# Kernel optimization log

Hardware: AMD Instinct MI355X
Metric: run time of the kernel (lower is better)

## Reference

```python
import jax, jax.numpy as jnp
import numpy as np
import math

# Instant-NGP hash-grid encoding constants (from HashEncodingConfig)
L = 16          # number of levels
LOG_T = 19
T = 2 ** LOG_T  # hash table size per level
F = 2           # features per entry
N_MIN = 16
N_MAX = 512
X_MIN = 0.0
X_MAX = 1.0
P = 2 ** 21     # number of query points

_scaler = math.exp((math.log(N_MAX) - math.log(N_MIN)) / (L - 1))
RESOLUTIONS = [int(N_MIN * _scaler ** i) for i in range(L)]

# 8 corner offsets of a voxel, shape [8, 3]
CORNER_OFFS = np.array([[i, j, k] for i in (0, 1) for j in (0, 1) for k in (0, 1)], dtype=np.int32)
# spatial hashing primes (tiny-cuda-nn / Instant-NGP)
PRIMES = np.array([1, 2654435761, 805459861], dtype=np.uint32)


def setup_inputs() -> dict:
    key = jax.random.key(0)
    kx, kh = jax.random.split(key)
    x = jax.random.uniform(kx, (P, 3), dtype=jnp.float32)  # points in [0,1]^3
    hashmap = jax.random.normal(kh, (L, T, F), dtype=jnp.float32) * 1e-4
    return {"x": x, "hashmap": hashmap}


def _encode_level(x, table, res):
    # x: [P,3] in [0,1]; table: [T,F]; res: python int
    xs = x * res                              # [P,3]
    xi = jnp.floor(xs).astype(jnp.int32)      # [P,3] integer cell
    xf = xs - xi.astype(xs.dtype)             # [P,3] fractional part
    corners = (xi[:, None, :] + CORNER_OFFS[None]).astype(jnp.uint32)  # [P,8,3]
    h = (corners[..., 0] * PRIMES[0]) ^ (corners[..., 1] * PRIMES[1]) ^ (corners[..., 2] * PRIMES[2])
    idx = (h & jnp.uint32(T - 1)).astype(jnp.int32)                     # [P,8]
    feats = table[idx]                                                  # [P,8,F] gather
    # trilinear weights: prod over 3 dims of xf (offset=1) or 1-xf (offset=0)
    w = jnp.prod(jnp.where(CORNER_OFFS[None].astype(bool), xf[:, None, :], 1.0 - xf[:, None, :]), axis=-1)  # [P,8]
    return jnp.sum(feats * w[..., None], axis=1)                        # [P,F]


def reference(x, hashmap):
    xn = (x - X_MIN) / (X_MAX - X_MIN)
    outs = [_encode_level(xn, hashmap[l], RESOLUTIONS[l]) for l in range(L)]
    return jnp.concatenate(outs, axis=-1)  # [P, L*F]
```

## Files before the change

kernel.cpp:

```cpp
#include <hip/hip_runtime.h>
#include <cstdint>
#include <cstddef>

namespace {
constexpr int kL = 16;
constexpr uint32_t kT = 1u << 19;
constexpr uint32_t kTmask = kT - 1u;
constexpr uint32_t kP1 = 2654435761u;
constexpr uint32_t kP2 = 805459861u;
}

struct Prep {
    uint32_t idx[8];
    float w[8];
};

__device__ __forceinline__ void prep_point(float px, float py, float pz,
                                           float fres, Prep& pr) {
    const float xs0 = px * fres;
    const float xs1 = py * fres;
    const float xs2 = pz * fres;
    const float fl0 = floorf(xs0);
    const float fl1 = floorf(xs1);
    const float fl2 = floorf(xs2);
    const float fx = xs0 - fl0;
    const float fy = xs1 - fl1;
    const float fz = xs2 - fl2;
    const uint32_t i0 = (uint32_t)(int)fl0;
    const uint32_t i1 = (uint32_t)(int)fl1;
    const uint32_t i2 = (uint32_t)(int)fl2;

    const uint32_t h0a = i0;
    const uint32_t h0b = i0 + 1u;
    const uint32_t h1a = i1 * kP1;
    const uint32_t h1b = (i1 + 1u) * kP1;
    const uint32_t h2a = i2 * kP2;
    const uint32_t h2b = (i2 + 1u) * kP2;

    pr.idx[0] = (h0a ^ h1a ^ h2a) & kTmask;
    pr.idx[1] = (h0a ^ h1a ^ h2b) & kTmask;
    pr.idx[2] = (h0a ^ h1b ^ h2a) & kTmask;
    pr.idx[3] = (h0a ^ h1b ^ h2b) & kTmask;
    pr.idx[4] = (h0b ^ h1a ^ h2a) & kTmask;
    pr.idx[5] = (h0b ^ h1a ^ h2b) & kTmask;
    pr.idx[6] = (h0b ^ h1b ^ h2a) & kTmask;
    pr.idx[7] = (h0b ^ h1b ^ h2b) & kTmask;

    const float wx0 = 1.0f - fx, wx1 = fx;
    const float wy0 = 1.0f - fy, wy1 = fy;
    const float wz0 = 1.0f - fz, wz1 = fz;
    pr.w[0] = wx0 * wy0 * wz0;
    pr.w[1] = wx0 * wy0 * wz1;
    pr.w[2] = wx0 * wy1 * wz0;
    pr.w[3] = wx0 * wy1 * wz1;
    pr.w[4] = wx1 * wy0 * wz0;
    pr.w[5] = wx1 * wy0 * wz1;
    pr.w[6] = wx1 * wy1 * wz0;
    pr.w[7] = wx1 * wy1 * wz1;
}

__device__ __forceinline__ uint32_t f32_to_bf16_rne(float f) {
    const uint32_t u = __float_as_uint(f);
    return (u + 0x7fffu + ((u >> 16) & 1u)) >> 16;
}

__global__ __launch_bounds__(256) void convert_tables(
    const float4* __restrict__ hm4,
    uint2* __restrict__ tbl_bf,
    int npairs)
{
    const int i = blockIdx.x * 256 + threadIdx.x;
    if (i >= npairs) return;
    const float4 v = hm4[i];
    uint2 o;
    o.x = (f32_to_bf16_rne(v.y) << 16) | f32_to_bf16_rne(v.x);
    o.y = (f32_to_bf16_rne(v.w) << 16) | f32_to_bf16_rne(v.z);
    tbl_bf[i] = o;
}

__global__ __launch_bounds__(256) void hashgrid_levels(
    const float* __restrict__ x,
    const uint32_t* __restrict__ tbl_bf,
    uint32_t* __restrict__ wsb,
    int P, int blocksPerLevel)
{
    const int l = blockIdx.x / blocksPerLevel;
    const int b = blockIdx.x - l * blocksPerLevel;
    const int t = b * 256 + threadIdx.x;
    const int p0 = 2 * t;
    if (p0 >= P) return;

    const int oct = (l * 11) >> 5;
    const int rem = l - 3 * oct;
    const float base = (float)(16 << oct);
    const float cmul = (rem == 0) ? 1.0f : ((rem == 1) ? 1.2599210499f : 1.5874010520f);
    const float fres = (float)(int)(base * cmul);

    const float* __restrict__ xp = x + (size_t)p0 * 3;
    const float ax = xp[0], ay = xp[1], az = xp[2];
    const float bx = xp[3], by = xp[4], bz = xp[5];

    Prep A, B;
    prep_point(ax, ay, az, fres, A);
    prep_point(bx, by, bz, fres, B);

    const uint32_t* __restrict__ tbl = tbl_bf + (size_t)l * (size_t)kT;

    uint32_t ua[8], ub[8];
#pragma unroll
    for (int c = 0; c < 8; ++c) ua[c] = tbl[A.idx[c]];
#pragma unroll
    for (int c = 0; c < 8; ++c) ub[c] = tbl[B.idx[c]];

    float a0 = 0.0f, a1 = 0.0f, b0 = 0.0f, b1 = 0.0f;
#pragma unroll
    for (int c = 0; c < 8; ++c) {
        a0 = fmaf(A.w[c], __uint_as_float(ua[c] << 16), a0);
        a1 = fmaf(A.w[c], __uint_as_float(ua[c] & 0xffff0000u), a1);
        b0 = fmaf(B.w[c], __uint_as_float(ub[c] << 16), b0);
        b1 = fmaf(B.w[c], __uint_as_float(ub[c] & 0xffff0000u), b1);
    }

    const uint32_t pa = (f32_to_bf16_rne(a1) << 16) | f32_to_bf16_rne(a0);
    const uint32_t pb = (f32_to_bf16_rne(b1) << 16) | f32_to_bf16_rne(b0);

    uint32_t* dst = wsb + (size_t)l * (size_t)P + (size_t)p0;
    if (p0 + 1 < P) {
        *reinterpret_cast<uint2*>(dst) = make_uint2(pa, pb);
    } else {
        *dst = pa;
    }
}

__global__ __launch_bounds__(256) void hashgrid_transpose(
    const uint32_t* __restrict__ wsb,
    float4* __restrict__ out4,
    int P)
{
    __shared__ uint32_t lds[256 * 17];
    const int tid = threadIdx.x;
    const int base = blockIdx.x * 256;

#pragma unroll
    for (int l = 0; l < kL; ++l) {
        const int p = base + tid;
        const uint32_t v = (p < P) ? wsb[(size_t)l * (size_t)P + (size_t)p] : 0u;
        lds[tid * 17 + l] = v;
    }
    __syncthreads();

    const int nvec = min(P - base, 256) * 8;
#pragma unroll
    for (int j = 0; j < 8; ++j) {
        const int tvec = j * 256 + tid;
        if (tvec < nvec) {
            const int pl = tvec >> 3;
            const int m = tvec & 7;
            const uint32_t ua = lds[pl * 17 + 2 * m];
            const uint32_t ub = lds[pl * 17 + 2 * m + 1];
            out4[(size_t)base * 8 + (size_t)tvec] =
                make_float4(__uint_as_float(ua << 16),
                            __uint_as_float(ua & 0xffff0000u),
                            __uint_as_float(ub << 16),
                            __uint_as_float(ub & 0xffff0000u));
        }
    }
}

__global__ __launch_bounds__(256) void hashgrid_fwd_mono(
    const float* __restrict__ x,
    const float* __restrict__ hashmap,
    float4* __restrict__ out4,
    int P)
{
    constexpr int RES[16] = {16, 20, 25, 32, 40, 50, 64, 80,
                             101, 128, 161, 203, 256, 322, 406, 512};
    const int p = blockIdx.x * 256 + threadIdx.x;
    if (p >= P) return;
    const float px = x[p * 3 + 0];
    const float py = x[p * 3 + 1];
    const float pz = x[p * 3 + 2];
    float acc[32];
#pragma unroll
    for (int l = 0; l < kL; ++l) {
        Prep pr;
        prep_point(px, py, pz, (float)RES[l], pr);
        const float2* __restrict__ tbl =
            reinterpret_cast<const float2*>(hashmap) + (size_t)l * (size_t)kT;
        float2 f[8];
#pragma unroll
        for (int c = 0; c < 8; ++c) f[c] = tbl[pr.idx[c]];
        float a0 = 0.0f, a1 = 0.0f;
#pragma unroll
        for (int c = 0; c < 8; ++c) {
            a0 = fmaf(pr.w[c], f[c].x, a0);
            a1 = fmaf(pr.w[c], f[c].y, a1);
        }
        acc[2 * l + 0] = a0;
        acc[2 * l + 1] = a1;
    }
    float4* __restrict__ dst = out4 + (size_t)p * 8;
#pragma unroll
    for (int j = 0; j < 8; ++j) {
        dst[j] = make_float4(acc[4 * j + 0], acc[4 * j + 1],
                             acc[4 * j + 2], acc[4 * j + 3]);
    }
}

extern "C" void kernel_launch(void* const* d_in, const int* in_sizes, int n_in,
                              void* d_out, int out_size, void* d_ws, size_t ws_size,
                              hipStream_t stream) {
    const float* x = (const float*)d_in[0];
    const float* hashmap = (const float*)d_in[1];
    float4* out4 = (float4*)d_out;

    const int P = in_sizes[0] / 3;
    const int block = 256;
    const int grid_p = (P + block - 1) / block;

    const size_t tbl_bytes = (size_t)kL * (size_t)kT * 4u;
    const size_t wsb_bytes = (size_t)kL * (size_t)P * sizeof(uint32_t);
    if (ws_size < tbl_bytes + wsb_bytes) {
        hashgrid_fwd_mono<<<grid_p, block, 0, stream>>>(x, hashmap, out4, P);
        return;
    }

    uint32_t* tbl_bf = (uint32_t*)d_ws;
    uint32_t* wsb = (uint32_t*)((char*)d_ws + tbl_bytes);

    const int npairs = (int)((size_t)kL * (size_t)kT / 2);
    convert_tables<<<(npairs + block - 1) / block, block, 0, stream>>>(
        (const float4*)hashmap, (uint2*)tbl_bf, npairs);

    const int blocksPerLevel = ((P + 1) / 2 + block - 1) / block;
    hashgrid_levels<<<kL * blocksPerLevel, block, 0, stream>>>(
        x, tbl_bf, wsb, P, blocksPerLevel);

    hashgrid_transpose<<<grid_p, block, 0, stream>>>(wsb, out4, P);
}
```

Baseline: 975.6 us.

## Materialize dense per-level grids for coarse levels to replace hashed gathers

For the eight coarsest levels, small prebuilt kernels materialize the hashed table into a dense voxel-indexed array. Levels 0-6 store z-adjacent corner pairs as uint2, so each point needs four 8-byte loads instead of eight scattered ones. Level 7 uses a plain dense (R+1)^3 array. The goal is better locality and fewer gather transactions for coarse levels. The cost is eight extra build launches and more workspace, and the main kernel now branches on a per-level mode passed in a parameter struct.

```diff
diff --git a/kernel.cpp b/kernel.cpp
--- a/kernel.cpp
+++ b/kernel.cpp
@@ -8,55 +8,17 @@
 constexpr uint32_t kTmask = kT - 1u;
 constexpr uint32_t kP1 = 2654435761u;
 constexpr uint32_t kP2 = 805459861u;
-}
-
-struct Prep {
-    uint32_t idx[8];
-    float w[8];
-};
-
-__device__ __forceinline__ void prep_point(float px, float py, float pz,
-                                           float fres, Prep& pr) {
-    const float xs0 = px * fres;
-    const float xs1 = py * fres;
-    const float xs2 = pz * fres;
-    const float fl0 = floorf(xs0);
-    const float fl1 = floorf(xs1);
-    const float fl2 = floorf(xs2);
-    const float fx = xs0 - fl0;
-    const float fy = xs1 - fl1;
-    const float fz = xs2 - fl2;
-    const uint32_t i0 = (uint32_t)(int)fl0;
-    const uint32_t i1 = (uint32_t)(int)fl1;
-    const uint32_t i2 = (uint32_t)(int)fl2;
-
-    const uint32_t h0a = i0;
-    const uint32_t h0b = i0 + 1u;
-    const uint32_t h1a = i1 * kP1;
-    const uint32_t h1b = (i1 + 1u) * kP1;
-    const uint32_t h2a = i2 * kP2;
-    const uint32_t h2b = (i2 + 1u) * kP2;
-
-    pr.idx[0] = (h0a ^ h1a ^ h2a) & kTmask;
-    pr.idx[1] = (h0a ^ h1a ^ h2b) & kTmask;
-    pr.idx[2] = (h0a ^ h1b ^ h2a) & kTmask;
-    pr.idx[3] = (h0a ^ h1b ^ h2b) & kTmask;
-    pr.idx[4] = (h0b ^ h1a ^ h2a) & kTmask;
-    pr.idx[5] = (h0b ^ h1a ^ h2b) & kTmask;
-    pr.idx[6] = (h0b ^ h1b ^ h2a) & kTmask;
-    pr.idx[7] = (h0b ^ h1b ^ h2b) & kTmask;
-
-    const float wx0 = 1.0f - fx, wx1 = fx;
-    const float wy0 = 1.0f - fy, wy1 = fy;
-    const float wz0 = 1.0f - fz, wz1 = fz;
-    pr.w[0] = wx0 * wy0 * wz0;
-    pr.w[1] = wx0 * wy0 * wz1;
-    pr.w[2] = wx0 * wy1 * wz0;
-    pr.w[3] = wx0 * wy1 * wz1;
-    pr.w[4] = wx1 * wy0 * wz0;
-    pr.w[5] = wx1 * wy0 * wz1;
-    pr.w[6] = wx1 * wy1 * wz0;
-    pr.w[7] = wx1 * wy1 * wz1;
+
+constexpr int kRES[16] = {16, 20, 25, 32, 40, 50, 64, 80,
+                          101, 128, 161, 203, 256, 322, 406, 512};
+
+constexpr int MODE_HASH = 0;
+constexpr int MODE_DENSE1 = 1;
+constexpr int MODE_DENSE2 = 2;
+}
+
+__device__ __forceinline__ uint32_t hash3(uint32_t c0, uint32_t c1, uint32_t c2) {
+    return (c0 ^ (c1 * kP1) ^ (c2 * kP2)) & kTmask;
 }
 
 __device__ __forceinline__ uint32_t f32_to_bf16_rne(float f) {
@@ -64,10 +26,11 @@
     return (u + 0x7fffu + ((u >> 16) & 1u)) >> 16;
 }
 
+__device__ __forceinline__ float bfx(uint32_t u) { return __uint_as_float(u << 16); }
+__device__ __forceinline__ float bfy(uint32_t u) { return __uint_as_float(u & 0xffff0000u); }
+
 __global__ __launch_bounds__(256) void convert_tables(
-    const float4* __restrict__ hm4,
-    uint2* __restrict__ tbl_bf,
-    int npairs)
+    const float4* __restrict__ hm4, uint2* __restrict__ tbl_bf, int npairs)
 {
     const int i = blockIdx.x * 256 + threadIdx.x;
     if (i >= npairs) return;
@@ -78,11 +41,51 @@
     tbl_bf[i] = o;
 }
 
+template <int R, int LVL>
+__global__ __launch_bounds__(256) void build_dense2(
+    const uint32_t* __restrict__ tbl_bf, uint2* __restrict__ d2)
+{
+    const int n = (R + 1) * (R + 1) * R;
+    const int s = blockIdx.x * 256 + threadIdx.x;
+    if (s >= n) return;
+    const int c2 = s % R;
+    const int t = s / R;
+    const int c1 = t % (R + 1);
+    const int c0 = t / (R + 1);
+    const uint32_t* tbl = tbl_bf + (size_t)LVL * (size_t)kT;
+    uint2 o;
+    o.x = tbl[hash3((uint32_t)c0, (uint32_t)c1, (uint32_t)c2)];
+    o.y = tbl[hash3((uint32_t)c0, (uint32_t)c1, (uint32_t)(c2 + 1))];
+    d2[s] = o;
+}
+
+template <int R, int LVL>
+__global__ __launch_bounds__(256) void build_dense1(
+    const uint32_t* __restrict__ tbl_bf, uint32_t* __restrict__ d1)
+{
+    const int n = (R + 1) * (R + 1) * (R + 1);
+    const int s = blockIdx.x * 256 + threadIdx.x;
+    if (s >= n) return;
+    const int c2 = s % (R + 1);
+    const int t = s / (R + 1);
+    const int c1 = t % (R + 1);
+    const int c0 = t / (R + 1);
+    const uint32_t* tbl = tbl_bf + (size_t)LVL * (size_t)kT;
+    d1[s] = tbl[hash3((uint32_t)c0, (uint32_t)c1, (uint32_t)c2)];
+}
+
+struct Params16 {
+    int mode[16];
+    int res[16];
+    float fres[16];
+    unsigned long long off[16];
+};
+
 __global__ __launch_bounds__(256) void hashgrid_levels(
     const float* __restrict__ x,
-    const uint32_t* __restrict__ tbl_bf,
+    const char* __restrict__ wsbase,
     uint32_t* __restrict__ wsb,
-    int P, int blocksPerLevel)
+    int P, int blocksPerLevel, Params16 prm)
 {
     const int l = blockIdx.x / blocksPerLevel;
     const int b = blockIdx.x - l * blocksPerLevel;
@@ -90,40 +93,149 @@
     const int p0 = 2 * t;
     if (p0 >= P) return;
 
-    const int oct = (l * 11) >> 5;
-    const int rem = l - 3 * oct;
-    const float base = (float)(16 << oct);
-    const float cmul = (rem == 0) ? 1.0f : ((rem == 1) ? 1.2599210499f : 1.5874010520f);
-    const float fres = (float)(int)(base * cmul);
+    const int mode = prm.mode[l];
+    const int R = prm.res[l];
+    const float fres = prm.fres[l];
+    const char* tblb = wsbase + prm.off[l];
 
     const float* __restrict__ xp = x + (size_t)p0 * 3;
-    const float ax = xp[0], ay = xp[1], az = xp[2];
-    const float bx = xp[3], by = xp[4], bz = xp[5];
-
-    Prep A, B;
-    prep_point(ax, ay, az, fres, A);
-    prep_point(bx, by, bz, fres, B);
-
-    const uint32_t* __restrict__ tbl = tbl_bf + (size_t)l * (size_t)kT;
-
-    uint32_t ua[8], ub[8];
-#pragma unroll
-    for (int c = 0; c < 8; ++c) ua[c] = tbl[A.idx[c]];
-#pragma unroll
-    for (int c = 0; c < 8; ++c) ub[c] = tbl[B.idx[c]];
+    const float axx = xp[0], ayy = xp[1], azz = xp[2];
+    const float bxx = xp[3], byy = xp[4], bzz = xp[5];
 
     float a0 = 0.0f, a1 = 0.0f, b0 = 0.0f, b1 = 0.0f;
-#pragma unroll
-    for (int c = 0; c < 8; ++c) {
-        a0 = fmaf(A.w[c], __uint_as_float(ua[c] << 16), a0);
-        a1 = fmaf(A.w[c], __uint_as_float(ua[c] & 0xffff0000u), a1);
-        b0 = fmaf(B.w[c], __uint_as_float(ub[c] << 16), b0);
-        b1 = fmaf(B.w[c], __uint_as_float(ub[c] & 0xffff0000u), b1);
-    }
+
+#define GEOM(px, py, pz, i0, i1, i2, fx, fy, fz)                       \
+    const float xs0 = (px) * fres, xs1 = (py) * fres, xs2 = (pz) * fres; \
+    const float fl0 = floorf(xs0), fl1 = floorf(xs1), fl2 = floorf(xs2); \
+    const float fx = xs0 - fl0, fy = xs1 - fl1, fz = xs2 - fl2;          \
+    const int i0 = (int)fl0, i1 = (int)fl1, i2 = (int)fl2;
+
+    if (mode == MODE_DENSE2) {
+        const uint2* __restrict__ d2 = reinterpret_cast<const uint2*>(tblb);
+        const int strideB = R;
+        const int strideA = R * (R + 1);
+        {
+            GEOM(axx, ayy, azz, i0, i1, i2, fx, fy, fz)
+            const int base = (i0 * (R + 1) + i1) * R + i2;
+            const uint2 u00 = d2[base];
+            const uint2 u01 = d2[base + strideB];
+            const uint2 u10 = d2[base + strideA];
+            const uint2 u11 = d2[base + strideA + strideB];
+            const float wx0 = 1.0f - fx, wx1 = fx;
+            const float wy0 = 1.0f - fy, wy1 = fy;
+            const float wz0 = 1.0f - fz, wz1 = fz;
+            float wab;
+            wab = wx0 * wy0;
+            a0 = fmaf(wab * wz0, bfx(u00.x), a0); a1 = fmaf(wab * wz0, bfy(u00.x), a1);
+            a0 = fmaf(wab * wz1, bfx(u00.y), a0); a1 = fmaf(wab * wz1, bfy(u00.y), a1);
+            wab = wx0 * wy1;
+            a0 = fmaf(wab * wz0, bfx(u01.x), a0); a1 = fmaf(wab * wz0, bfy(u01.x), a1);
+            a0 = fmaf(wab * wz1, bfx(u01.y), a0); a1 = fmaf(wab * wz1, bfy(u01.y), a1);
+            wab = wx1 * wy0;
+            a0 = fmaf(wab * wz0, bfx(u10.x), a0); a1 = fmaf(wab * wz0, bfy(u10.x), a1);
+            a0 = fmaf(wab * wz1, bfx(u10.y), a0); a1 = fmaf(wab * wz1, bfy(u10.y), a1);
+            wab = wx1 * wy1;
+            a0 = fmaf(wab * wz0, bfx(u11.x), a0); a1 = fmaf(wab * wz0, bfy(u11.x), a1);
+            a0 = fmaf(wab * wz1, bfx(u11.y), a0); a1 = fmaf(wab * wz1, bfy(u11.y), a1);
+        }
+        {
+            GEOM(bxx, byy, bzz, i0, i1, i2, fx, fy, fz)
+            const int base = (i0 * (R + 1) + i1) * R + i2;
+            const uint2 u00 = d2[base];
+            const uint2 u01 = d2[base + strideB];
+            const uint2 u10 = d2[base + strideA];
+            const uint2 u11 = d2[base + strideA + strideB];
+            const float wx0 = 1.0f - fx, wx1 = fx;
+            const float wy0 = 1.0f - fy, wy1 = fy;
+            const float wz0 = 1.0f - fz, wz1 = fz;
+            float wab;
+            wab = wx0 * wy0;
+            b0 = fmaf(wab * wz0, bfx(u00.x), b0); b1 = fmaf(wab * wz0, bfy(u00.x), b1);
+            b0 = fmaf(wab * wz1, bfx(u00.y), b0); b1 = fmaf(wab * wz1, bfy(u00.y), b1);
+            wab = wx0 * wy1;
+            b0 = fmaf(wab * wz0, bfx(u01.x), b0); b1 = fmaf(wab * wz0, bfy(u01.x), b1);
+            b0 = fmaf(wab * wz1, bfx(u01.y), b0); b1 = fmaf(wab * wz1, bfy(u01.y), b1);
+            wab = wx1 * wy0;
+            b0 = fmaf(wab * wz0, bfx(u10.x), b0); b1 = fmaf(wab * wz0, bfy(u10.x), b1);
+            b0 = fmaf(wab * wz1, bfx(u10.y), b0); b1 = fmaf(wab * wz1, bfy(u10.y), b1);
+            wab = wx1 * wy1;
+            b0 = fmaf(wab * wz0, bfx(u11.x), b0); b1 = fmaf(wab * wz0, bfy(u11.x), b1);
+            b0 = fmaf(wab * wz1, bfx(u11.y), b0); b1 = fmaf(wab * wz1, bfy(u11.y), b1);
+        }
+    } else {
+        const uint32_t* __restrict__ tbl = reinterpret_cast<const uint32_t*>(tblb);
+        uint32_t ia[8], ib[8];
+        float wa[8], wb[8];
+        {
+            GEOM(axx, ayy, azz, i0, i1, i2, fx, fy, fz)
+            if (mode == MODE_DENSE1) {
+                const int base = (i0 * (R + 1) + i1) * (R + 1) + i2;
+                const int sB = R + 1, sA = (R + 1) * (R + 1);
+                ia[0] = base;          ia[1] = base + 1;
+                ia[2] = base + sB;     ia[3] = base + sB + 1;
+                ia[4] = base + sA;     ia[5] = base + sA + 1;
+                ia[6] = base + sA + sB; ia[7] = base + sA + sB + 1;
+            } else {
+                const uint32_t h0a = (uint32_t)i0, h0b = (uint32_t)i0 + 1u;
+                const uint32_t h1a = (uint32_t)i1 * kP1, h1b = ((uint32_t)i1 + 1u) * kP1;
+                const uint32_t h2a = (uint32_t)i2 * kP2, h2b = ((uint32_t)i2 + 1u) * kP2;
+                ia[0] = (h0a ^ h1a ^ h2a) & kTmask; ia[1] = (h0a ^ h1a ^ h2b) & kTmask;
+                ia[2] = (h0a ^ h1b ^ h2a) & kTmask; ia[3] = (h0a ^ h1b ^ h2b) & kTmask;
+                ia[4] = (h0b ^ h1a ^ h2a) & kTmask; ia[5] = (h0b ^ h1a ^ h2b) & kTmask;
+                ia[6] = (h0b ^ h1b ^ h2a) & kTmask; ia[7] = (h0b ^ h1b ^ h2b) & kTmask;
+            }
+            const float wx0 = 1.0f - fx, wx1 = fx;
+            const float wy0 = 1.0f - fy, wy1 = fy;
+            const float wz0 = 1.0f - fz, wz1 = fz;
+            wa[0] = wx0 * wy0 * wz0; wa[1] = wx0 * wy0 * wz1;
+            wa[2] = wx0 * wy1 * wz0; wa[3] = wx0 * wy1 * wz1;
+            wa[4] = wx1 * wy0 * wz0; wa[5] = wx1 * wy0 * wz1;
+            wa[6] = wx1 * wy1 * wz0; wa[7] = wx1 * wy1 * wz1;
+        }
+        {
+            GEOM(bxx, byy, bzz, i0, i1, i2, fx, fy, fz)
+            if (mode == MODE_DENSE1) {
+                const int base = (i0 * (R + 1) + i1) * (R + 1) + i2;
+                const int sB = R + 1, sA = (R + 1) * (R + 1);
+                ib[0] = base;          ib[1] = base + 1;
+                ib[2] = base + sB;     ib[3] = base + sB + 1;
+                ib[4] = base + sA;     ib[5] = base + sA + 1;
+                ib[6] = base + sA + sB; ib[7] = base + sA + sB + 1;
+            } else {
+                const uint32_t h0a = (uint32_t)i0, h0b = (uint32_t)i0 + 1u;
+                const uint32_t h1a = (uint32_t)i1 * kP1, h1b = ((uint32_t)i1 + 1u) * kP1;
+                const uint32_t h2a = (uint32_t)i2 * kP2, h2b = ((uint32_t)i2 + 1u) * kP2;
+                ib[0] = (h0a ^ h1a ^ h2a) & kTmask; ib[1] = (h0a ^ h1a ^ h2b) & kTmask;
+                ib[2] = (h0a ^ h1b ^ h2a) & kTmask; ib[3] = (h0a ^ h1b ^ h2b) & kTmask;
+                ib[4] = (h0b ^ h1a ^ h2a) & kTmask; ib[5] = (h0b ^ h1a ^ h2b) & kTmask;
+                ib[6] = (h0b ^ h1b ^ h2a) & kTmask; ib[7] = (h0b ^ h1b ^ h2b) & kTmask;
+            }
+            const float wx0 = 1.0f - fx, wx1 = fx;
+            const float wy0 = 1.0f - fy, wy1 = fy;
+            const float wz0 = 1.0f - fz, wz1 = fz;
+            wb[0] = wx0 * wy0 * wz0; wb[1] = wx0 * wy0 * wz1;
+            wb[2] = wx0 * wy1 * wz0; wb[3] = wx0 * wy1 * wz1;
+            wb[4] = wx1 * wy0 * wz0; wb[5] = wx1 * wy0 * wz1;
+            wb[6] = wx1 * wy1 * wz0; wb[7] = wx1 * wy1 * wz1;
+        }
+
+        uint32_t ua[8], ub[8];
+#pragma unroll
+        for (int c = 0; c < 8; ++c) ua[c] = tbl[ia[c]];
+#pragma unroll
+        for (int c = 0; c < 8; ++c) ub[c] = tbl[ib[c]];
+#pragma unroll
+        for (int c = 0; c < 8; ++c) {
+            a0 = fmaf(wa[c], bfx(ua[c]), a0);
+            a1 = fmaf(wa[c], bfy(ua[c]), a1);
+            b0 = fmaf(wb[c], bfx(ub[c]), b0);
+            b1 = fmaf(wb[c], bfy(ub[c]), b1);
+        }
+    }
+#undef GEOM
 
     const uint32_t pa = (f32_to_bf16_rne(a1) << 16) | f32_to_bf16_rne(a0);
     const uint32_t pb = (f32_to_bf16_rne(b1) << 16) | f32_to_bf16_rne(b0);
-
     uint32_t* dst = wsb + (size_t)l * (size_t)P + (size_t)p0;
     if (p0 + 1 < P) {
         *reinterpret_cast<uint2*>(dst) = make_uint2(pa, pb);
@@ -133,9 +245,7 @@
 }
 
 __global__ __launch_bounds__(256) void hashgrid_transpose(
-    const uint32_t* __restrict__ wsb,
-    float4* __restrict__ out4,
-    int P)
+    const uint32_t* __restrict__ wsb, float4* __restrict__ out4, int P)
 {
     __shared__ uint32_t lds[256 * 17];
     const int tid = threadIdx.x;
@@ -159,52 +269,58 @@
             const uint32_t ua = lds[pl * 17 + 2 * m];
             const uint32_t ub = lds[pl * 17 + 2 * m + 1];
             out4[(size_t)base * 8 + (size_t)tvec] =
-                make_float4(__uint_as_float(ua << 16),
-                            __uint_as_float(ua & 0xffff0000u),
-                            __uint_as_float(ub << 16),
-                            __uint_as_float(ub & 0xffff0000u));
+                make_float4(bfx(ua), bfy(ua), bfx(ub), bfy(ub));
         }
     }
 }
 
 __global__ __launch_bounds__(256) void hashgrid_fwd_mono(
-    const float* __restrict__ x,
-    const float* __restrict__ hashmap,
-    float4* __restrict__ out4,
-    int P)
-{
-    constexpr int RES[16] = {16, 20, 25, 32, 40, 50, 64, 80,
-                             101, 128, 161, 203, 256, 322, 406, 512};
+    const float* __restrict__ x, const float* __restrict__ hashmap,
+    float4* __restrict__ out4, int P)
+{
     const int p = blockIdx.x * 256 + threadIdx.x;
     if (p >= P) return;
-    const float px = x[p * 3 + 0];
-    const float py = x[p * 3 + 1];
-    const float pz = x[p * 3 + 2];
+    const float px = x[p * 3 + 0], py = x[p * 3 + 1], pz = x[p * 3 + 2];
     float acc[32];
 #pragma unroll
     for (int l = 0; l < kL; ++l) {
-        Prep pr;
-        prep_point(px, py, pz, (float)RES[l], pr);
-        const float2* __restrict__ tbl =
-            reinterpret_cast<const float2*>(hashmap) + (size_t)l * (size_t)kT;
+        const float fres = (float)kRES[l];
+        const float xs0 = px * fres, xs1 = py * fres, xs2 = pz * fres;
+        const float fl0 = floorf(xs0), fl1 = floorf(xs1), fl2 = floorf(xs2);
+        const float fx = xs0 - fl0, fy = xs1 - fl1, fz = xs2 - fl2;
+        const uint32_t i0 = (uint32_t)(int)fl0, i1 = (uint32_t)(int)fl1, i2 = (uint32_t)(int)fl2;
+        const uint32_t h0a = i0, h0b = i0 + 1u;
+        const uint32_t h1a = i1 * kP1, h1b = (i1 + 1u) * kP1;
+        const uint32_t h2a = i2 * kP2, h2b = (i2 + 1u) * kP2;
+        uint32_t idx[8];
+        idx[0] = (h0a ^ h1a ^ h2a) & kTmask; idx[1] = (h0a ^ h1a ^ h2b) & kTmask;
+        idx[2] = (h0a ^ h1b ^ h2a) & kTmask; idx[3] = (h0a ^ h1b ^ h2b) & kTmask;
+        idx[4] = (h0b ^ h1a ^ h2a) & kTmask; idx[5] = (h0b ^ h1a ^ h2b) & kTmask;
+        idx[6] = (h0b ^ h1b ^ h2a) & kTmask; idx[7] = (h0b ^ h1b ^ h2b) & kTmask;
+        const float2* tbl = reinterpret_cast<const float2*>(hashmap) + (size_t)l * kT;
         float2 f[8];
 #pragma unroll
-        for (int c = 0; c < 8; ++c) f[c] = tbl[pr.idx[c]];
+        for (int c = 0; c < 8; ++c) f[c] = tbl[idx[c]];
+        const float wx0 = 1.0f - fx, wx1 = fx;
+        const float wy0 = 1.0f - fy, wy1 = fy;
+        const float wz0 = 1.0f - fz, wz1 = fz;
+        float w[8];
+        w[0] = wx0 * wy0 * wz0; w[1] = wx0 * wy0 * wz1;
+        w[2] = wx0 * wy1 * wz0; w[3] = wx0 * wy1 * wz1;
+        w[4] = wx1 * wy0 * wz0; w[5] = wx1 * wy0 * wz1;
+        w[6] = wx1 * wy1 * wz0; w[7] = wx1 * wy1 * wz1;
         float a0 = 0.0f, a1 = 0.0f;
 #pragma unroll
         for (int c = 0; c < 8; ++c) {
-            a0 = fmaf(pr.w[c], f[c].x, a0);
-            a1 = fmaf(pr.w[c], f[c].y, a1);
-        }
-        acc[2 * l + 0] = a0;
-        acc[2 * l + 1] = a1;
-    }
-    float4* __restrict__ dst = out4 + (size_t)p * 8;
-#pragma unroll
-    for (int j = 0; j < 8; ++j) {
-        dst[j] = make_float4(acc[4 * j + 0], acc[4 * j + 1],
-                             acc[4 * j + 2], acc[4 * j + 3]);
-    }
+            a0 = fmaf(w[c], f[c].x, a0);
+            a1 = fmaf(w[c], f[c].y, a1);
+        }
+        acc[2 * l + 0] = a0; acc[2 * l + 1] = a1;
+    }
+    float4* dst = out4 + (size_t)p * 8;
+#pragma unroll
+    for (int j = 0; j < 8; ++j)
+        dst[j] = make_float4(acc[4 * j], acc[4 * j + 1], acc[4 * j + 2], acc[4 * j + 3]);
 }
 
 extern "C" void kernel_launch(void* const* d_in, const int* in_sizes, int n_in,
@@ -219,22 +335,52 @@
     const int grid_p = (P + block - 1) / block;
 
     const size_t tbl_bytes = (size_t)kL * (size_t)kT * 4u;
-    const size_t wsb_bytes = (size_t)kL * (size_t)P * sizeof(uint32_t);
-    if (ws_size < tbl_bytes + wsb_bytes) {
+    size_t dense_off[8];
+    size_t cur = tbl_bytes;
+    for (int l = 0; l < 8; ++l) {
+        const size_t R = (size_t)kRES[l];
+        const size_t bytes = (l < 7) ? (R + 1) * (R + 1) * R * 8
+                                     : (R + 1) * (R + 1) * (R + 1) * 4;
+        cur = (cur + 255) & ~(size_t)255;
+        dense_off[l] = cur;
+        cur += bytes;
+    }
+    cur = (cur + 255) & ~(size_t)255;
+    const size_t wsb_off = cur;
+    const size_t need = wsb_off + (size_t)kL * (size_t)P * 4u;
+    if (ws_size < need) {
         hashgrid_fwd_mono<<<grid_p, block, 0, stream>>>(x, hashmap, out4, P);
         return;
     }
 
-    uint32_t* tbl_bf = (uint32_t*)d_ws;
-    uint32_t* wsb = (uint32_t*)((char*)d_ws + tbl_bytes);
+    char* wsc = (char*)d_ws;
+    uint32_t* tbl_bf = (uint32_t*)wsc;
+    uint32_t* wsb = (uint32_t*)(wsc + wsb_off);
 
     const int npairs = (int)((size_t)kL * (size_t)kT / 2);
     convert_tables<<<(npairs + block - 1) / block, block, 0, stream>>>(
         (const float4*)hashmap, (uint2*)tbl_bf, npairs);
 
+#define BUILD2(R, L) build_dense2<R, L><<<(((R+1)*(R+1)*R) + 255) / 256, 256, 0, stream>>>( \
+        tbl_bf, (uint2*)(wsc + dense_off[L]))
+    BUILD2(16, 0); BUILD2(20, 1); BUILD2(25, 2); BUILD2(32, 3);
+    BUILD2(40, 4); BUILD2(50, 5); BUILD2(64, 6);
+#undef BUILD2
+    build_dense1<80, 7><<<((81 * 81 * 81) + 255) / 256, 256, 0, stream>>>(
+        tbl_bf, (uint32_t*)(wsc + dense_off[7]));
+
+    Params16 prm;
+    for (int l = 0; l < kL; ++l) {
+        prm.res[l] = kRES[l];
+        prm.fres[l] = (float)kRES[l];
+        if (l < 7)      { prm.mode[l] = MODE_DENSE2; prm.off[l] = dense_off[l]; }
+        else if (l == 7){ prm.mode[l] = MODE_DENSE1; prm.off[l] = dense_off[l]; }
+        else            { prm.mode[l] = MODE_HASH;
+                          prm.off[l] = (size_t)l * (size_t)kT * 4u; }
+    }
     const int blocksPerLevel = ((P + 1) / 2 + block - 1) / block;
     hashgrid_levels<<<kL * blocksPerLevel, block, 0, stream>>>(
-        x, tbl_bf, wsb, P, blocksPerLevel);
+        x, wsc, wsb, P, blocksPerLevel, prm);
 
     hashgrid_transpose<<<grid_p, block, 0, stream>>>(wsb, out4, P);
 }
```

Result: faster. 881.3 us (-9.7%).
